# Optimization experiments

Measured on AMD Instinct MI355X. Metric: run time of the kernel, lower is better.

Reference implementation:

```python
import jax, jax.numpy as jnp
import numpy as np

WINDOW_SIZE = 11
PAD = WINDOW_SIZE // 2


def _box_filter(x):
    """Depthwise uniform box filter, separable: two 1D convs with 1/W weights.

    x: [N, C, H, W] float. Zero padding of PAD on each side (matches torch
    F.conv2d(padding=PAD) with the outer-product uniform window).
    """
    c = x.shape[1]
    w = jnp.full((c, 1, WINDOW_SIZE, 1), 1.0 / WINDOW_SIZE, dtype=x.dtype)
    # vertical pass
    y = jax.lax.conv_general_dilated(
        x, w, window_strides=(1, 1), padding=((PAD, PAD), (0, 0)),
        dimension_numbers=('NCHW', 'OIHW', 'NCHW'), feature_group_count=c)
    # horizontal pass
    w2 = jnp.transpose(w, (0, 1, 3, 2))  # [C,1,1,WINDOW_SIZE]
    y = jax.lax.conv_general_dilated(
        y, w2, window_strides=(1, 1), padding=((0, 0), (PAD, PAD)),
        dimension_numbers=('NCHW', 'OIHW', 'NCHW'), feature_group_count=c)
    return y


def _ssim_loss(img1, img2):
    C1 = 0.01 ** 2
    C2 = 0.03 ** 2
    mu1 = _box_filter(img1)
    mu2 = _box_filter(img2)
    mu1_sq = mu1 * mu1
    mu2_sq = mu2 * mu2
    mu1_mu2 = mu1 * mu2
    sigma1_sq = _box_filter(img1 * img1) - mu1_sq
    sigma2_sq = _box_filter(img2 * img2) - mu2_sq
    sigma12 = _box_filter(img1 * img2) - mu1_mu2
    ssim_map = ((2 * mu1_mu2 + C1) * (2 * sigma12 + C2)) / (
        (mu1_sq + mu2_sq + C1) * (sigma1_sq + sigma2_sq + C2))
    return 1.0 - jnp.mean(ssim_map)


def setup_inputs() -> dict:
    key = jax.random.key(0)
    k1, k2 = jax.random.split(key)
    shape = (16, 3, 512, 512)
    img1 = jax.random.uniform(k1, shape, dtype=jnp.float32)
    img2 = jax.random.uniform(k2, shape, dtype=jnp.float32)
    return {"img1": img1, "img2": img2}


def reference(img1, img2):
    return _ssim_loss(img1, img2)
```

## Files before the change

kernel.cpp:

```cpp
#include <hip/hip_runtime.h>
#include <math.h>


typedef __fp16 half2_t __attribute__((ext_vector_type(2)));
typedef __fp16 half4_t __attribute__((ext_vector_type(4)));

constexpr int WIN  = 11;
constexpr int OTW  = 116;
constexpr int OTH  = 32;
constexpr int VP   = 127;
constexpr int SEGR = 8;
constexpr int SEGI = SEGR + WIN - 1;
constexpr int GPW  = 15;
constexpr int H = 512, W = 512;
constexpr int NPLANES = 16 * 3;
constexpr int GRIDX = (W + OTW - 1) / OTW;
constexpr long long NPIX = (long long)NPLANES * H * W;

__device__ __forceinline__ float ssim_px(float ws, float wd, float wss, float wdd) {
    const float C1 = 1e-4f;
    const float C2 = 9e-4f;
    const float k1 = 1.0f / 121.0f;
    const float c2a = 0.5f * k1 * k1;
    const float c2c = 0.5f * k1;
    const float P = (c2a * ws) * ws;
    const float Q = (c2a * wd) * wd;
    const float U = c2c * wss;
    const float T = c2c * wdd;
    const float r1 = P - Q;
    const float p1 = P + Q;
    const float t1 = U - T;
    const float u1 = U + T;
    const float num = (r1 + C1) * (t1 - r1 + C2);
    const float den = (p1 + C1) * (u1 - p1 + C2);
    return num * __builtin_amdgcn_rcpf(den);
}

__device__ __forceinline__ float ssim4(half4_t a) {
    return ssim_px((float)a[0], (float)a[1], (float)a[2], (float)a[3]);
}

template<bool XE, bool YE>
__device__ __forceinline__ void vpass(const float* __restrict__ ca,
                                      const float* __restrict__ cb,
                                      int gy0, bool xok0, bool xok1,
                                      int vrow0, int lane,
                                      half4_t (*V)[VP]) {
    float2 va[SEGI], vb[SEGI];
#pragma unroll
    for (int r = 0; r < SEGI; ++r) {
        if (YE) {
            const int gy = gy0 + r;
            if ((unsigned)gy < (unsigned)H) {
                va[r] = *(const float2*)(ca + (size_t)gy * W);
                vb[r] = *(const float2*)(cb + (size_t)gy * W);
            } else {
                va[r] = make_float2(0.f, 0.f);
                vb[r] = make_float2(0.f, 0.f);
            }
        } else {
            va[r] = *(const float2*)(ca + (size_t)(gy0 + r) * W);
            vb[r] = *(const float2*)(cb + (size_t)(gy0 + r) * W);
        }
    }

    half2_t r0[WIN], r1[WIN];
    half2_t asd0 = {(__fp16)0, (__fp16)0}, asq0 = asd0;
    half2_t asd1 = asd0, asq1 = asd0;
#pragma unroll
    for (int r = 0; r < SEGI; ++r) {
        float a0 = va[r].x, a1 = va[r].y, b0 = vb[r].x, b1 = vb[r].y;
        if (XE) {
            a0 = xok0 ? a0 : 0.f;  b0 = xok0 ? b0 : 0.f;
            a1 = xok1 ? a1 : 0.f;  b1 = xok1 ? b1 : 0.f;
        }
        const int i = r % WIN;
        const half2_t p0 = __builtin_amdgcn_cvt_pkrtz(a0 + b0, a0 - b0);
        const half2_t p1 = __builtin_amdgcn_cvt_pkrtz(a1 + b1, a1 - b1);
        asd0 += p0;  asq0 += p0 * p0;
        asd1 += p1;  asq1 += p1 * p1;
        if (r >= WIN) {
            const half2_t o0 = r0[i], o1 = r1[i];
            asd0 -= o0;  asq0 -= o0 * o0;
            asd1 -= o1;  asq1 -= o1 * o1;
        }
        r0[i] = p0;  r1[i] = p1;
        if (r >= WIN - 1) {
            const int vr = vrow0 + r - (WIN - 1);
            const half4_t v0 = {asd0[0], asd0[1], asq0[0], asq0[1]};
            const half4_t v1 = {asd1[0], asd1[1], asq1[0], asq1[1]};
            V[vr][2 * lane]     = v0;
            V[vr][2 * lane + 1] = v1;
        }
    }
}

template<bool CHK>
__device__ __forceinline__ float hpass(const half4_t (*V)[VP], int row,
                                       int x0, int gxb) {
    half4_t acc = {(__fp16)0, (__fp16)0, (__fp16)0, (__fp16)0};
#pragma unroll
    for (int r = 0; r < WIN; ++r)
        acc += V[row][x0 + 1 + r];
    float local = 0.0f;
    if (!CHK || gxb < W)
        local = ssim4(acc);
#pragma unroll
    for (int k = 1; k < GPW; ++k) {
        acc += V[row][x0 + k + WIN] - V[row][x0 + k];
        if ((x0 + k < OTW) && (!CHK || gxb + k < W))
            local += ssim4(acc);
    }
    return local;
}

__global__ __launch_bounds__(256, 4)
void ssim_tile_kernel(const float* __restrict__ img1,
                      const float* __restrict__ img2,
                      float* __restrict__ partials) {
    __shared__ half4_t V[OTH][VP];
    __shared__ float wsum[4];

    const int tid  = threadIdx.x;
    const int wave = tid >> 6;
    const int lane = tid & 63;
    const int tx0 = blockIdx.x * OTW;
    const int ty0 = blockIdx.y * OTH;
    const int plane = blockIdx.z;
    const float* __restrict__ pa = img1 + (size_t)plane * H * W;
    const float* __restrict__ pb = img2 + (size_t)plane * H * W;

    {
        const int gxl = tx0 - 6 + 2 * lane;
        const bool xok0 = (unsigned)gxl < (unsigned)W;
        const bool xok1 = (unsigned)(gxl + 1) < (unsigned)W;
        const int gc = min(max(gxl, 0), W - 2);
        const int gy0 = ty0 + wave * SEGR - (WIN / 2);
        const int vrow0 = wave * SEGR;
        const bool xe = (blockIdx.x == 0) || (blockIdx.x == GRIDX - 1);
        const bool ye = (gy0 < 0) || (gy0 + SEGI > H);
        const float* __restrict__ ca = pa + gc;
        const float* __restrict__ cb = pb + gc;
        if (!xe) {
            if (!ye) vpass<false, false>(ca, cb, gy0, xok0, xok1, vrow0, lane, V);
            else     vpass<false, true >(ca, cb, gy0, xok0, xok1, vrow0, lane, V);
        } else {
            if (!ye) vpass<true, false>(ca, cb, gy0, xok0, xok1, vrow0, lane, V);
            else     vpass<true, true >(ca, cb, gy0, xok0, xok1, vrow0, lane, V);
        }
    }
    __syncthreads();

    const int row = tid & 31;
    const int x0  = (tid >> 5) * GPW;
    const int gxb = tx0 + x0;
    float local;
    if (blockIdx.x != GRIDX - 1)
        local = hpass<false>(V, row, x0, gxb);
    else
        local = hpass<true >(V, row, x0, gxb);

    for (int off = 32; off > 0; off >>= 1)
        local += __shfl_down(local, off);
    if (lane == 0) wsum[wave] = local;
    __syncthreads();
    if (tid == 0) {
        const int bid = (blockIdx.z * gridDim.y + blockIdx.y) * gridDim.x + blockIdx.x;
        partials[bid] = wsum[0] + wsum[1] + wsum[2] + wsum[3];
    }
}

__global__ __launch_bounds__(1024)
void ssim_reduce_kernel(const float4* __restrict__ partials4, int n4,
                        float* __restrict__ out) {
    double s = 0.0;
    for (int i = threadIdx.x; i < n4; i += 1024) {
        const float4 p = partials4[i];
        s += (double)p.x + (double)p.y + (double)p.z + (double)p.w;
    }
    for (int off = 32; off > 0; off >>= 1)
        s += __shfl_down(s, off);
    __shared__ double wsum[16];
    if ((threadIdx.x & 63) == 0) wsum[threadIdx.x >> 6] = s;
    __syncthreads();
    if (threadIdx.x == 0) {
        double total = 0.0;
        for (int w = 0; w < 16; ++w) total += wsum[w];
        out[0] = (float)(1.0 - total / (double)NPIX);
    }
}

extern "C" void kernel_launch(void* const* d_in, const int* in_sizes, int n_in,
                              void* d_out, int out_size, void* d_ws, size_t ws_size,
                              hipStream_t stream) {
    const float* img1 = (const float*)d_in[0];
    const float* img2 = (const float*)d_in[1];
    float* out = (float*)d_out;
    float* partials = (float*)d_ws;

    dim3 grid(GRIDX, H / OTH, NPLANES);
    dim3 block(256);
    ssim_tile_kernel<<<grid, block, 0, stream>>>(img1, img2, partials);

    const int nblocks = GRIDX * (H / OTH) * NPLANES;
    ssim_reduce_kernel<<<1, 1024, 0, stream>>>((const float4*)partials,
                                               nblocks / 4, out);
}
```

Before: 34.14 us.

## Shrink tile blocks to a single wavefront covering eight output rows

Each block becomes a single 64-thread wavefront that computes an 8-row tile, replacing 256-thread blocks of four waves covering 32 rows. The shared-memory intermediate shrinks to 8 rows, and the cross-wave LDS reduction and its second barrier go away. The grid grows fourfold, so more partials are written and the single-block reduce kernel has more to sum. The launch bounds change to allow more resident blocks per CU.

```diff
diff --git a/kernel.cpp b/kernel.cpp
--- a/kernel.cpp
+++ b/kernel.cpp
@@ -7,7 +7,6 @@
 
 constexpr int WIN  = 11;
 constexpr int OTW  = 116;
-constexpr int OTH  = 32;
 constexpr int VP   = 127;
 constexpr int SEGR = 8;
 constexpr int SEGI = SEGR + WIN - 1;
@@ -44,8 +43,7 @@
 __device__ __forceinline__ void vpass(const float* __restrict__ ca,
                                       const float* __restrict__ cb,
                                       int gy0, bool xok0, bool xok1,
-                                      int vrow0, int lane,
-                                      half4_t (*V)[VP]) {
+                                      int lane, half4_t* __restrict__ V) {
     float2 va[SEGI], vb[SEGI];
 #pragma unroll
     for (int r = 0; r < SEGI; ++r) {
@@ -86,46 +84,44 @@
         }
         r0[i] = p0;  r1[i] = p1;
         if (r >= WIN - 1) {
-            const int vr = vrow0 + r - (WIN - 1);
+            const int vr = r - (WIN - 1);
             const half4_t v0 = {asd0[0], asd0[1], asq0[0], asq0[1]};
             const half4_t v1 = {asd1[0], asd1[1], asq1[0], asq1[1]};
-            V[vr][2 * lane]     = v0;
-            V[vr][2 * lane + 1] = v1;
+            V[vr * VP + 2 * lane]     = v0;
+            V[vr * VP + 2 * lane + 1] = v1;
         }
     }
 }
 
 template<bool CHK>
-__device__ __forceinline__ float hpass(const half4_t (*V)[VP], int row,
+__device__ __forceinline__ float hpass(const half4_t* __restrict__ V, int row,
                                        int x0, int gxb) {
     half4_t acc = {(__fp16)0, (__fp16)0, (__fp16)0, (__fp16)0};
+    const half4_t* __restrict__ vr = V + row * VP;
 #pragma unroll
     for (int r = 0; r < WIN; ++r)
-        acc += V[row][x0 + 1 + r];
+        acc += vr[x0 + 1 + r];
     float local = 0.0f;
     if (!CHK || gxb < W)
         local = ssim4(acc);
 #pragma unroll
     for (int k = 1; k < GPW; ++k) {
-        acc += V[row][x0 + k + WIN] - V[row][x0 + k];
+        acc += vr[x0 + k + WIN] - vr[x0 + k];
         if ((x0 + k < OTW) && (!CHK || gxb + k < W))
             local += ssim4(acc);
     }
     return local;
 }
 
-__global__ __launch_bounds__(256, 4)
+__global__ __launch_bounds__(64, 5)
 void ssim_tile_kernel(const float* __restrict__ img1,
                       const float* __restrict__ img2,
                       float* __restrict__ partials) {
-    __shared__ half4_t V[OTH][VP];
-    __shared__ float wsum[4];
-
-    const int tid  = threadIdx.x;
-    const int wave = tid >> 6;
-    const int lane = tid & 63;
+    __shared__ half4_t V[SEGR * VP + 8];
+
+    const int lane = threadIdx.x;
     const int tx0 = blockIdx.x * OTW;
-    const int ty0 = blockIdx.y * OTH;
+    const int ty0 = blockIdx.y * SEGR;
     const int plane = blockIdx.z;
     const float* __restrict__ pa = img1 + (size_t)plane * H * W;
     const float* __restrict__ pb = img2 + (size_t)plane * H * W;
@@ -135,24 +131,23 @@
         const bool xok0 = (unsigned)gxl < (unsigned)W;
         const bool xok1 = (unsigned)(gxl + 1) < (unsigned)W;
         const int gc = min(max(gxl, 0), W - 2);
-        const int gy0 = ty0 + wave * SEGR - (WIN / 2);
-        const int vrow0 = wave * SEGR;
+        const int gy0 = ty0 - (WIN / 2);
         const bool xe = (blockIdx.x == 0) || (blockIdx.x == GRIDX - 1);
         const bool ye = (gy0 < 0) || (gy0 + SEGI > H);
         const float* __restrict__ ca = pa + gc;
         const float* __restrict__ cb = pb + gc;
         if (!xe) {
-            if (!ye) vpass<false, false>(ca, cb, gy0, xok0, xok1, vrow0, lane, V);
-            else     vpass<false, true >(ca, cb, gy0, xok0, xok1, vrow0, lane, V);
+            if (!ye) vpass<false, false>(ca, cb, gy0, xok0, xok1, lane, V);
+            else     vpass<false, true >(ca, cb, gy0, xok0, xok1, lane, V);
         } else {
-            if (!ye) vpass<true, false>(ca, cb, gy0, xok0, xok1, vrow0, lane, V);
-            else     vpass<true, true >(ca, cb, gy0, xok0, xok1, vrow0, lane, V);
+            if (!ye) vpass<true, false>(ca, cb, gy0, xok0, xok1, lane, V);
+            else     vpass<true, true >(ca, cb, gy0, xok0, xok1, lane, V);
         }
     }
     __syncthreads();
 
-    const int row = tid & 31;
-    const int x0  = (tid >> 5) * GPW;
+    const int row = lane >> 3;
+    const int x0  = (lane & 7) * GPW;
     const int gxb = tx0 + x0;
     float local;
     if (blockIdx.x != GRIDX - 1)
@@ -162,11 +157,9 @@
 
     for (int off = 32; off > 0; off >>= 1)
         local += __shfl_down(local, off);
-    if (lane == 0) wsum[wave] = local;
-    __syncthreads();
-    if (tid == 0) {
+    if (lane == 0) {
         const int bid = (blockIdx.z * gridDim.y + blockIdx.y) * gridDim.x + blockIdx.x;
-        partials[bid] = wsum[0] + wsum[1] + wsum[2] + wsum[3];
+        partials[bid] = local;
     }
 }
 
@@ -198,11 +191,11 @@
     float* out = (float*)d_out;
     float* partials = (float*)d_ws;
 
-    dim3 grid(GRIDX, H / OTH, NPLANES);
-    dim3 block(256);
+    dim3 grid(GRIDX, H / SEGR, NPLANES);
+    dim3 block(64);
     ssim_tile_kernel<<<grid, block, 0, stream>>>(img1, img2, partials);
 
-    const int nblocks = GRIDX * (H / OTH) * NPLANES;
+    const int nblocks = GRIDX * (H / SEGR) * NPLANES;
     ssim_reduce_kernel<<<1, 1024, 0, stream>>>((const float4*)partials,
                                                nblocks / 4, out);
 }
```

New measurement: 51.40 us. 50.6% more time.

## Halve SSIM tile width to one column per lane with higher occupancy

Applied to the files above, without the earlier changes.

Narrows the output tile from 116 to 53 columns so each lane handles a single input column with scalar loads instead of float2 pairs. Per-thread register state in the vertical pass is halved, the shared buffer is roughly halved, and the launch bound is raised from 4 to 8 blocks per SM to get more waves resident. The cost is more halo overhead: the 10-column horizontal halo is now re-read relative to 53 outputs instead of 116, giving more redundant global loads and more blocks overall.

```diff
diff --git a/kernel.cpp b/kernel.cpp
--- a/kernel.cpp
+++ b/kernel.cpp
@@ -6,12 +6,12 @@
 typedef __fp16 half4_t __attribute__((ext_vector_type(4)));
 
 constexpr int WIN  = 11;
-constexpr int OTW  = 116;
+constexpr int OTW  = 53;
 constexpr int OTH  = 32;
-constexpr int VP   = 127;
+constexpr int VP   = 65;
 constexpr int SEGR = 8;
 constexpr int SEGI = SEGR + WIN - 1;
-constexpr int GPW  = 15;
+constexpr int GPW  = 7;
 constexpr int H = 512, W = 512;
 constexpr int NPLANES = 16 * 3;
 constexpr int GRIDX = (W + OTW - 1) / OTW;
@@ -43,82 +43,76 @@
 template<bool XE, bool YE>
 __device__ __forceinline__ void vpass(const float* __restrict__ ca,
                                       const float* __restrict__ cb,
-                                      int gy0, bool xok0, bool xok1,
-                                      int vrow0, int lane,
-                                      half4_t (*V)[VP]) {
-    float2 va[SEGI], vb[SEGI];
+                                      int gy0, bool xok, int lane,
+                                      half4_t* __restrict__ V) {
+    float va[SEGI], vb[SEGI];
 #pragma unroll
     for (int r = 0; r < SEGI; ++r) {
         if (YE) {
             const int gy = gy0 + r;
             if ((unsigned)gy < (unsigned)H) {
-                va[r] = *(const float2*)(ca + (size_t)gy * W);
-                vb[r] = *(const float2*)(cb + (size_t)gy * W);
+                va[r] = ca[(size_t)gy * W];
+                vb[r] = cb[(size_t)gy * W];
             } else {
-                va[r] = make_float2(0.f, 0.f);
-                vb[r] = make_float2(0.f, 0.f);
+                va[r] = 0.f;
+                vb[r] = 0.f;
             }
         } else {
-            va[r] = *(const float2*)(ca + (size_t)(gy0 + r) * W);
-            vb[r] = *(const float2*)(cb + (size_t)(gy0 + r) * W);
-        }
-    }
-
-    half2_t r0[WIN], r1[WIN];
-    half2_t asd0 = {(__fp16)0, (__fp16)0}, asq0 = asd0;
-    half2_t asd1 = asd0, asq1 = asd0;
+            va[r] = ca[(size_t)(gy0 + r) * W];
+            vb[r] = cb[(size_t)(gy0 + r) * W];
+        }
+    }
+
+    half2_t ring[WIN];
+    half2_t asd = {(__fp16)0, (__fp16)0}, asq = asd;
 #pragma unroll
     for (int r = 0; r < SEGI; ++r) {
-        float a0 = va[r].x, a1 = va[r].y, b0 = vb[r].x, b1 = vb[r].y;
+        float a = va[r], b = vb[r];
         if (XE) {
-            a0 = xok0 ? a0 : 0.f;  b0 = xok0 ? b0 : 0.f;
-            a1 = xok1 ? a1 : 0.f;  b1 = xok1 ? b1 : 0.f;
+            a = xok ? a : 0.f;
+            b = xok ? b : 0.f;
         }
         const int i = r % WIN;
-        const half2_t p0 = __builtin_amdgcn_cvt_pkrtz(a0 + b0, a0 - b0);
-        const half2_t p1 = __builtin_amdgcn_cvt_pkrtz(a1 + b1, a1 - b1);
-        asd0 += p0;  asq0 += p0 * p0;
-        asd1 += p1;  asq1 += p1 * p1;
+        const half2_t p = __builtin_amdgcn_cvt_pkrtz(a + b, a - b);
+        asd += p;  asq += p * p;
         if (r >= WIN) {
-            const half2_t o0 = r0[i], o1 = r1[i];
-            asd0 -= o0;  asq0 -= o0 * o0;
-            asd1 -= o1;  asq1 -= o1 * o1;
-        }
-        r0[i] = p0;  r1[i] = p1;
+            const half2_t o = ring[i];
+            asd -= o;  asq -= o * o;
+        }
+        ring[i] = p;
         if (r >= WIN - 1) {
-            const int vr = vrow0 + r - (WIN - 1);
-            const half4_t v0 = {asd0[0], asd0[1], asq0[0], asq0[1]};
-            const half4_t v1 = {asd1[0], asd1[1], asq1[0], asq1[1]};
-            V[vr][2 * lane]     = v0;
-            V[vr][2 * lane + 1] = v1;
+            const int vr = r - (WIN - 1);
+            const half4_t v = {asd[0], asd[1], asq[0], asq[1]};
+            V[vr * VP + lane] = v;
         }
     }
 }
 
 template<bool CHK>
-__device__ __forceinline__ float hpass(const half4_t (*V)[VP], int row,
+__device__ __forceinline__ float hpass(const half4_t* __restrict__ V, int row,
                                        int x0, int gxb) {
+    const half4_t* __restrict__ vr = V + row * VP;
     half4_t acc = {(__fp16)0, (__fp16)0, (__fp16)0, (__fp16)0};
 #pragma unroll
-    for (int r = 0; r < WIN; ++r)
-        acc += V[row][x0 + 1 + r];
+    for (int j = 0; j < WIN; ++j)
+        acc += vr[x0 + j];
     float local = 0.0f;
-    if (!CHK || gxb < W)
+    if (x0 < OTW && (!CHK || gxb < W))
         local = ssim4(acc);
 #pragma unroll
     for (int k = 1; k < GPW; ++k) {
-        acc += V[row][x0 + k + WIN] - V[row][x0 + k];
+        acc += vr[x0 + k + WIN - 1] - vr[x0 + k - 1];
         if ((x0 + k < OTW) && (!CHK || gxb + k < W))
             local += ssim4(acc);
     }
     return local;
 }
 
-__global__ __launch_bounds__(256, 4)
+__global__ __launch_bounds__(256, 8)
 void ssim_tile_kernel(const float* __restrict__ img1,
                       const float* __restrict__ img2,
                       float* __restrict__ partials) {
-    __shared__ half4_t V[OTH][VP];
+    __shared__ half4_t V[OTH * VP + 16];
     __shared__ float wsum[4];
 
     const int tid  = threadIdx.x;
@@ -131,22 +125,21 @@
     const float* __restrict__ pb = img2 + (size_t)plane * H * W;
 
     {
-        const int gxl = tx0 - 6 + 2 * lane;
-        const bool xok0 = (unsigned)gxl < (unsigned)W;
-        const bool xok1 = (unsigned)(gxl + 1) < (unsigned)W;
-        const int gc = min(max(gxl, 0), W - 2);
+        const int gx  = tx0 - 5 + lane;
+        const bool xok = (unsigned)gx < (unsigned)W;
+        const int gc  = min(max(gx, 0), W - 1);
         const int gy0 = ty0 + wave * SEGR - (WIN / 2);
-        const int vrow0 = wave * SEGR;
         const bool xe = (blockIdx.x == 0) || (blockIdx.x == GRIDX - 1);
         const bool ye = (gy0 < 0) || (gy0 + SEGI > H);
         const float* __restrict__ ca = pa + gc;
         const float* __restrict__ cb = pb + gc;
+        half4_t* __restrict__ Vw = V + (wave * SEGR) * VP;
         if (!xe) {
-            if (!ye) vpass<false, false>(ca, cb, gy0, xok0, xok1, vrow0, lane, V);
-            else     vpass<false, true >(ca, cb, gy0, xok0, xok1, vrow0, lane, V);
+            if (!ye) vpass<false, false>(ca, cb, gy0, xok, lane, Vw);
+            else     vpass<false, true >(ca, cb, gy0, xok, lane, Vw);
         } else {
-            if (!ye) vpass<true, false>(ca, cb, gy0, xok0, xok1, vrow0, lane, V);
-            else     vpass<true, true >(ca, cb, gy0, xok0, xok1, vrow0, lane, V);
+            if (!ye) vpass<true, false>(ca, cb, gy0, xok, lane, Vw);
+            else     vpass<true, true >(ca, cb, gy0, xok, lane, Vw);
         }
     }
     __syncthreads();
```

New measurement: 43.68 us. 1.28x slower.
